# Performance work log

Measured on AMD Instinct MI355X. Metric: run time of the kernel, lower is better.

Reference implementation:

```python
import jax, jax.numpy as jnp
import numpy as np

N_USER = 50000
N_ITEM = 50000
N = N_USER + N_ITEM
NNZ = 3200000
EMB = 64
N_LAYERS = 3
BATCH = 4096
NEG_SLOPE = 0.2


def setup_inputs() -> dict:
    key = jax.random.key(0)
    ks = jax.random.split(key, 12)
    inp = {
        "users": jax.random.randint(ks[0], (BATCH,), 0, N_USER),
        "pos_items": jax.random.randint(ks[1], (BATCH,), 0, N_ITEM),
        "neg_items": jax.random.randint(ks[2], (BATCH,), 0, N_ITEM),
        "adj_row": jax.random.randint(ks[3], (NNZ,), 0, N),
        "adj_col": jax.random.randint(ks[4], (NNZ,), 0, N),
        # normalized adjacency values ~ 1/degree scale
        "adj_val": jax.random.uniform(ks[5], (NNZ,), dtype=jnp.float32) * (1.0 / 32.0),
        "user_emb": jax.random.normal(ks[6], (N_USER, EMB), dtype=jnp.float32) * 0.1,
        "item_emb": jax.random.normal(ks[7], (N_ITEM, EMB), dtype=jnp.float32) * 0.1,
        "W_gc": jax.random.normal(ks[8], (N_LAYERS, EMB, EMB), dtype=jnp.float32) * (1.0 / np.sqrt(EMB)),
        "b_gc": jax.random.normal(ks[9], (N_LAYERS, 1, EMB), dtype=jnp.float32) * 0.01,
        "W_bi": jax.random.normal(ks[10], (N_LAYERS, EMB, EMB), dtype=jnp.float32) * (1.0 / np.sqrt(EMB)),
        "b_bi": jax.random.normal(ks[11], (N_LAYERS, 1, EMB), dtype=jnp.float32) * 0.01,
    }
    return inp


def _spmm(adj_row, adj_col, adj_val, x):
    # sparse [N,N] @ dense [N,D] via gather + segment_sum
    msgs = adj_val[:, None] * x[adj_col]            # [nnz, D]
    return jax.ops.segment_sum(msgs, adj_row, num_segments=N)


def reference(users, pos_items, neg_items, adj_row, adj_col, adj_val,
              user_emb, item_emb, W_gc, b_gc, W_bi, b_bi):
    ego = jnp.concatenate([user_emb, item_emb], axis=0)   # [N, EMB]
    all_embs = [ego]
    for k in range(N_LAYERS):
        side = _spmm(adj_row, adj_col, adj_val, ego)      # [N, EMB]
        sum_emb = side @ W_gc[k] + b_gc[k]                # GC transform
        bi_emb = (ego * side) @ W_bi[k] + b_bi[k]         # BI transform
        ego = jax.nn.leaky_relu(sum_emb + bi_emb, negative_slope=NEG_SLOPE)
        # mess_dropout = 0 -> identity; L2 normalize rows (F.normalize, eps=1e-12)
        norm = jnp.maximum(jnp.linalg.norm(ego, axis=1, keepdims=True), 1e-12)
        all_embs.append(ego / norm)
    all_embs = jnp.concatenate(all_embs, axis=1)          # [N, EMB*(L+1)]
    u_g = all_embs[:N_USER]
    i_g = all_embs[N_USER:]
    return (u_g[users], i_g[pos_items], i_g[neg_items])
```

## Files before the change

### kernel.cpp

```cpp
#include <hip/hip_runtime.h>
#include <hip/hip_bf16.h>

#define N_USERC 50000
#define N_ITEMC 50000
#define NTOT    100000
#define NNZC    3200000
#define NGRP    (NNZC/4)
#define EMBC    64
#define BATCHC  4096
#define NSLOT   (3*BATCHC)
#define NBKT    196
#define CAP     17408
typedef unsigned long long u64;

typedef __attribute__((ext_vector_type(4))) float floatx4;
typedef __attribute__((ext_vector_type(2))) float floatx2;
typedef __attribute__((ext_vector_type(4))) int   intx4;
typedef __attribute__((ext_vector_type(2))) int   intx2;
typedef __attribute__((ext_vector_type(2))) unsigned uintx2;
typedef __attribute__((ext_vector_type(8))) short shortx8;

__device__ __forceinline__ float bf2f(unsigned short u) {
    return __int_as_float(((int)u) << 16);
}
__device__ __forceinline__ unsigned short f2bf(float f) {
    __hip_bfloat16 h = __float2bfloat16(f);
    return *(unsigned short*)&h;
}
__device__ __forceinline__ unsigned v2fix(float v) {
    int q = (int)(v * 1048576.0f + 0.5f);
    return (unsigned)min(q, 32767);
}

#define NB_INIT  (NTOT * EMBC / 4 / 256)
__global__ void k_prep(const float4* __restrict__ ue, const float4* __restrict__ ie,
                       ushort4* __restrict__ xb0,
                       const float* __restrict__ Wgc, const float* __restrict__ Wbi,
                       const float* __restrict__ bgc, const float* __restrict__ bbi,
                       unsigned short* __restrict__ wgT, unsigned short* __restrict__ wbT,
                       float* __restrict__ biasSum, int* __restrict__ gbcur) {
    __shared__ float wlds[64 * 65];
    int tid = threadIdx.x;
    if (blockIdx.x < NB_INIT) {
        long i = (long)blockIdx.x * 256 + tid;
        const long nu4 = (long)N_USERC * EMBC / 4;
        float4 v = (i < nu4) ? ue[i] : ie[i - nu4];
        ushort4 b; b.x = f2bf(v.x); b.y = f2bf(v.y); b.z = f2bf(v.z); b.w = f2bf(v.w);
        xb0[i] = b;
    } else if (blockIdx.x < NB_INIT + 6) {
        int wb = blockIdx.x - NB_INIT;
        int k = wb >> 1, m = wb & 1;
        const float* W = (m ? Wbi : Wgc) + k * 4096;
        unsigned short* WT = (m ? wbT : wgT) + k * 4096;
        #pragma unroll
        for (int it = 0; it < 4; ++it) {
            int i = it * 1024 + tid * 4;
            float4 v = *(const float4*)(W + i);
            int d = i >> 6, c = i & 63;
            wlds[d * 65 + c + 0] = v.x;
            wlds[d * 65 + c + 1] = v.y;
            wlds[d * 65 + c + 2] = v.z;
            wlds[d * 65 + c + 3] = v.w;
        }
        __syncthreads();
        int c = tid >> 2;
        int d0 = (tid & 3) * 16;
        unsigned short vals[16];
        #pragma unroll
        for (int j = 0; j < 16; ++j)
            vals[j] = f2bf(wlds[(d0 + j) * 65 + c]);
        *(uint4*)(WT + tid * 16)     = *(const uint4*)(vals);
        *(uint4*)(WT + tid * 16 + 8) = *(const uint4*)(vals + 8);
        if (m == 0 && tid < 64) biasSum[k * 64 + tid] = bgc[k * 64 + tid] + bbi[k * 64 + tid];
    } else {
        if (tid < NBKT) gbcur[tid] = tid * CAP;
    }
}

__global__ __launch_bounds__(256) void k_scatterP(const intx4* __restrict__ row4, const intx4* __restrict__ col4,
                                                  const floatx4* __restrict__ val4, int* __restrict__ gbcur,
                                                  u64* __restrict__ eb) {
    __shared__ int bh[NBKT], bbase[NBKT], bcur[NBKT];
    int tid = threadIdx.x;
    for (int i = tid; i < NBKT; i += 256) { bh[i] = 0; bcur[i] = 0; }
    __syncthreads();
    long gbase = (long)blockIdx.x * 1024;
    u64 e[16]; int bk[16];
    #pragma unroll
    for (int it = 0; it < 4; ++it) {
        long g = gbase + it * 256 + tid;
        if (g < NGRP) {
            intx4 r = __builtin_nontemporal_load(row4 + g);
            intx4 c = __builtin_nontemporal_load(col4 + g);
            floatx4 v = __builtin_nontemporal_load(val4 + g);
            e[it*4+0] = ((u64)r.x << 32) | ((u64)(unsigned)c.x << 15) | v2fix(v.x); bk[it*4+0] = r.x >> 9;
            e[it*4+1] = ((u64)r.y << 32) | ((u64)(unsigned)c.y << 15) | v2fix(v.y); bk[it*4+1] = r.y >> 9;
            e[it*4+2] = ((u64)r.z << 32) | ((u64)(unsigned)c.z << 15) | v2fix(v.z); bk[it*4+2] = r.z >> 9;
            e[it*4+3] = ((u64)r.w << 32) | ((u64)(unsigned)c.w << 15) | v2fix(v.w); bk[it*4+3] = r.w >> 9;
            atomicAdd(&bh[bk[it*4+0]], 1);
            atomicAdd(&bh[bk[it*4+1]], 1);
            atomicAdd(&bh[bk[it*4+2]], 1);
            atomicAdd(&bh[bk[it*4+3]], 1);
        } else {
            bk[it*4+0] = bk[it*4+1] = bk[it*4+2] = bk[it*4+3] = -1;
        }
    }
    __syncthreads();
    for (int i = tid; i < NBKT; i += 256)
        if (bh[i] > 0) bbase[i] = atomicAdd(&gbcur[i], bh[i]);
    __syncthreads();
    #pragma unroll
    for (int i = 0; i < 16; i++) {
        if (bk[i] >= 0) {
            int p = bbase[bk[i]] + atomicAdd(&bcur[bk[i]], 1);
            eb[p] = e[i];
        }
    }
}

__global__ __launch_bounds__(1024) void k_csrC(const u64* __restrict__ eb, const int* __restrict__ gbcur,
                                               intx2* __restrict__ rp2, unsigned* __restrict__ ecv) {
    __shared__ int lhist[512];
    __shared__ int lcur[512];
    __shared__ int sm[256];
    int b = blockIdx.x;
    int tid = threadIdx.x;
    int row0 = b << 9;
    if (tid < 512) lhist[tid] = 0;
    __syncthreads();
    int start = b * CAP;
    int end = gbcur[b];
    for (int e = start + tid; e < end; e += 1024) {
        u64 w = eb[e];
        int rl = (int)((w >> 32) & 0x1FFFF) - row0;
        atomicAdd(&lhist[rl], 1);
    }
    __syncthreads();
    int h0 = 0, h1 = 0, pair = 0;
    if (tid < 256) {
        h0 = lhist[2 * tid]; h1 = lhist[2 * tid + 1];
        pair = h0 + h1;
        sm[tid] = pair;
    }
    __syncthreads();
    for (int off = 1; off < 256; off <<= 1) {
        int u = 0;
        if (tid < 256 && tid >= off) u = sm[tid - off];
        __syncthreads();
        if (tid < 256) sm[tid] += u;
        __syncthreads();
    }
    if (tid < 256) {
        int pairExcl = sm[tid] - pair;
        int e0 = start + pairExcl;
        int e1 = e0 + h0;
        lcur[2 * tid] = e0;
        lcur[2 * tid + 1] = e1;
        int rg0 = row0 + 2 * tid, rg1 = rg0 + 1;
        if (rg0 < NTOT) { intx2 v; v.x = e0; v.y = e1; rp2[rg0] = v; }
        if (rg1 < NTOT) { intx2 v; v.x = e1; v.y = e1 + h1; rp2[rg1] = v; }
    }
    __syncthreads();
    for (int e = start + tid; e < end; e += 1024) {
        u64 w = eb[e];
        int rl = (int)((w >> 32) & 0x1FFFF) - row0;
        int p = atomicAdd(&lcur[rl], 1);
        ecv[p] = (unsigned)(w & 0xFFFFFFFFu);
    }
}

#define SPMM_BLOCKS 2048
__global__ __launch_bounds__(256) void k_spmm(const intx2* __restrict__ rp2, const unsigned* __restrict__ ecv,
                                              const unsigned short* __restrict__ xb,
                                              unsigned short* __restrict__ side_bf) {
    int wid = blockIdx.x * 4 + (threadIdx.x >> 6);
    int lane = threadIdx.x & 63;
    int q = lane >> 4;
    int t4 = (lane & 15) * 4;
    unsigned tb = (unsigned)(t4 * 2);
    const char* xbc = (const char*)xb;
    for (int r = wid; r < NTOT; r += SPMM_BLOCKS * 4) {
        intx2 se = rp2[r];
        int s = se.x;
        int len = se.y - s;
        const unsigned* ebase = ecv + s;
        floatx2 acc01 = {0.f, 0.f}, acc23 = {0.f, 0.f};

        int nfull = len >> 4;
        int j = 0;
        for (int it = 0; it < nfull; ++it, j += 16) {
            unsigned pk[4];
            #pragma unroll
            for (int u = 0; u < 4; ++u)
                pk[u] = __builtin_nontemporal_load(ebase + j + u * 4 + q);
            uintx2 xv[4];
            #pragma unroll
            for (int u = 0; u < 4; ++u)
                xv[u] = *(const uintx2*)(xbc + ((pk[u] >> 15) * 128u + tb));
            #pragma unroll
            for (int u = 0; u < 4; ++u) {
                float w = (float)(pk[u] & 0x7fffu);
                floatx2 x01, x23;
                x01.x = __uint_as_float(xv[u].x << 16);
                x01.y = __uint_as_float(xv[u].x & 0xffff0000u);
                x23.x = __uint_as_float(xv[u].y << 16);
                x23.y = __uint_as_float(xv[u].y & 0xffff0000u);
                acc01 += w * x01;
                acc23 += w * x23;
            }
        }
        if (j < len) {
            unsigned pk[4]; bool vm[4];
            #pragma unroll
            for (int u = 0; u < 4; ++u) {
                int je = j + u * 4 + q;
                vm[u] = (je < len);
                pk[u] = __builtin_nontemporal_load(ebase + (vm[u] ? je : 0));
            }
            uintx2 xv[4];
            #pragma unroll
            for (int u = 0; u < 4; ++u)
                xv[u] = *(const uintx2*)(xbc + ((pk[u] >> 15) * 128u + tb));
            #pragma unroll
            for (int u = 0; u < 4; ++u) {
                float w = vm[u] ? (float)(pk[u] & 0x7fffu) : 0.f;
                floatx2 x01, x23;
                x01.x = __uint_as_float(xv[u].x << 16);
                x01.y = __uint_as_float(xv[u].x & 0xffff0000u);
                x23.x = __uint_as_float(xv[u].y << 16);
                x23.y = __uint_as_float(xv[u].y & 0xffff0000u);
                acc01 += w * x01;
                acc23 += w * x23;
            }
        }

        float a0 = acc01.x, a1 = acc01.y, a2 = acc23.x, a3 = acc23.y;
        a0 += __shfl_xor(a0, 16); a1 += __shfl_xor(a1, 16); a2 += __shfl_xor(a2, 16); a3 += __shfl_xor(a3, 16);
        a0 += __shfl_xor(a0, 32); a1 += __shfl_xor(a1, 32); a2 += __shfl_xor(a2, 32); a3 += __shfl_xor(a3, 32);
        if (lane < 16) {
            const float SC = 1.0f / 1048576.0f;
            ushort4 o; o.x = f2bf(a0 * SC); o.y = f2bf(a1 * SC); o.z = f2bf(a2 * SC); o.w = f2bf(a3 * SC);
            *(ushort4*)(side_bf + (long)r * EMBC + t4) = o;
        }
    }
}

#define RPB 128
#define LDP 72
__global__ __launch_bounds__(256) void k_layer_mfma(
    const unsigned short* __restrict__ side_bf, const unsigned short* __restrict__ xb_in,
    unsigned short* __restrict__ xb_out,
    const unsigned short* __restrict__ wgT, const unsigned short* __restrict__ wbT,
    const float* __restrict__ biasSum)
{
    __shared__ unsigned short sS[RPB * LDP];
    __shared__ unsigned short sM[RPB * LDP];
    __shared__ unsigned short sWg[64 * LDP];
    __shared__ unsigned short sWb[64 * LDP];
    __shared__ float sBias[64];

    int tid = threadIdx.x;
    int row0 = blockIdx.x * RPB;

    #pragma unroll
    for (int it = 0; it < 2; ++it) {
        int item = it * 256 + tid;
        int c = item >> 3, ch = item & 7;
        *(uint4*)(sWg + c * LDP + ch * 8) = *(const uint4*)(wgT + c * 64 + ch * 8);
        *(uint4*)(sWb + c * LDP + ch * 8) = *(const uint4*)(wbT + c * 64 + ch * 8);
    }
    if (tid < 64) sBias[tid] = biasSum[tid];

    #pragma unroll
    for (int it = 0; it < (RPB * 8) / 256; ++it) {
        int item = it * 256 + tid;
        int r = item >> 3, ch = item & 7;
        long grow = row0 + r;
        uint4 sv = make_uint4(0, 0, 0, 0), ev = make_uint4(0, 0, 0, 0);
        if (grow < NTOT) {
            sv = *(const uint4*)(side_bf + grow * 64 + ch * 8);
            ev = *(const uint4*)(xb_in + grow * 64 + ch * 8);
        }
        uint4 mv;
        mv.x = f2bf(bf2f(ev.x & 0xffff) * bf2f(sv.x & 0xffff)) |
               ((unsigned int)f2bf(bf2f(ev.x >> 16) * bf2f(sv.x >> 16)) << 16);
        mv.y = f2bf(bf2f(ev.y & 0xffff) * bf2f(sv.y & 0xffff)) |
               ((unsigned int)f2bf(bf2f(ev.y >> 16) * bf2f(sv.y >> 16)) << 16);
        mv.z = f2bf(bf2f(ev.z & 0xffff) * bf2f(sv.z & 0xffff)) |
               ((unsigned int)f2bf(bf2f(ev.z >> 16) * bf2f(sv.z >> 16)) << 16);
        mv.w = f2bf(bf2f(ev.w & 0xffff) * bf2f(sv.w & 0xffff)) |
               ((unsigned int)f2bf(bf2f(ev.w >> 16) * bf2f(sv.w >> 16)) << 16);
        *(uint4*)(sS + r * LDP + ch * 8) = sv;
        *(uint4*)(sM + r * LDP + ch * 8) = mv;
    }
    __syncthreads();

    int wave = tid >> 6, lane = tid & 63;
    int quad = lane >> 4, l16 = lane & 15;

    floatx4 accG[2][4], accB[2][4];
    #pragma unroll
    for (int rt = 0; rt < 2; rt++)
        #pragma unroll
        for (int ct = 0; ct < 4; ct++) {
            accG[rt][ct] = (floatx4){0.f, 0.f, 0.f, 0.f};
            accB[rt][ct] = (floatx4){0.f, 0.f, 0.f, 0.f};
        }

    #pragma unroll
    for (int kc = 0; kc < 64; kc += 32) {
        shortx8 aS[2], aM[2];
        #pragma unroll
        for (int rt = 0; rt < 2; rt++) {
            int r = wave * 32 + rt * 16 + l16;
            aS[rt] = *(const shortx8*)(sS + r * LDP + kc + quad * 8);
            aM[rt] = *(const shortx8*)(sM + r * LDP + kc + quad * 8);
        }
        #pragma unroll
        for (int ct = 0; ct < 4; ct++) {
            int c = ct * 16 + l16;
            shortx8 bG = *(const shortx8*)(sWg + c * LDP + kc + quad * 8);
            shortx8 bB = *(const shortx8*)(sWb + c * LDP + kc + quad * 8);
            #pragma unroll
            for (int rt = 0; rt < 2; rt++) {
                accG[rt][ct] = __builtin_amdgcn_mfma_f32_16x16x32_bf16(aS[rt], bG, accG[rt][ct], 0, 0, 0);
                accB[rt][ct] = __builtin_amdgcn_mfma_f32_16x16x32_bf16(aM[rt], bB, accB[rt][ct], 0, 0, 0);
            }
        }
    }

    #pragma unroll
    for (int rt = 0; rt < 2; rt++)
        #pragma unroll
        for (int ct = 0; ct < 4; ct++) {
            int c = ct * 16 + l16;
            float bs = sBias[c];
            #pragma unroll
            for (int reg = 0; reg < 4; reg++) {
                int r = wave * 32 + rt * 16 + quad * 4 + reg;
                long grow = row0 + r;
                if (grow < NTOT) {
                    float v = accG[rt][ct][reg] + accB[rt][ct][reg] + bs;
                    float o = (v > 0.f) ? v : 0.2f * v;
                    xb_out[grow * 64 + c] = f2bf(o);
                }
            }
        }
}

__global__ __launch_bounds__(256) void k_gatherAll(
    const unsigned short* __restrict__ xb0, const unsigned short* __restrict__ xb1,
    const unsigned short* __restrict__ xb2, const unsigned short* __restrict__ xb3,
    const int* __restrict__ users, const int* __restrict__ pos, const int* __restrict__ neg,
    float* __restrict__ out) {
    int gw = (blockIdx.x * blockDim.x + threadIdx.x) >> 6;
    int lane = threadIdx.x & 63;
    int slot = gw >> 2, layer = gw & 3;
    if (slot >= NSLOT) return;
    int row;
    if (slot < BATCHC)          row = users[slot];
    else if (slot < 2 * BATCHC) row = N_USERC + pos[slot - BATCHC];
    else                        row = N_USERC + neg[slot - 2 * BATCHC];
    const unsigned short* src = (layer == 0) ? xb0 : (layer == 1) ? xb1 : (layer == 2) ? xb2 : xb3;
    float v = bf2f(src[(long)row * 64 + lane]);
    if (layer != 0) {
        float ss = v * v;
        for (int off = 32; off > 0; off >>= 1) ss += __shfl_xor(ss, off);
        float nrm = fmaxf(sqrtf(ss), 1e-12f);
        v = v / nrm;
    }
    out[(long)slot * 256 + layer * 64 + lane] = v;
}

extern "C" void kernel_launch(void* const* d_in, const int* in_sizes, int n_in,
                              void* d_out, int out_size, void* d_ws, size_t ws_size,
                              hipStream_t stream) {
    const int*   users   = (const int*)d_in[0];
    const int*   pos     = (const int*)d_in[1];
    const int*   neg     = (const int*)d_in[2];
    const int*   adj_row = (const int*)d_in[3];
    const int*   adj_col = (const int*)d_in[4];
    const float* adj_val = (const float*)d_in[5];
    const float* user_emb = (const float*)d_in[6];
    const float* item_emb = (const float*)d_in[7];
    const float* W_gc = (const float*)d_in[8];
    const float* b_gc = (const float*)d_in[9];
    const float* W_bi = (const float*)d_in[10];
    const float* b_bi = (const float*)d_in[11];
    float* out = (float*)d_out;

    char* p = (char*)d_ws;
    unsigned* ecv = (unsigned*)p;               p += (size_t)NBKT * CAP * 4;
    u64*  eb  = (u64*)p;                        p += (size_t)NBKT * CAP * 8;
    unsigned short* xb2 = (unsigned short*)eb;
    unsigned short* xb3 = (unsigned short*)((char*)eb + (size_t)NTOT * EMBC * 2);
    unsigned short* side_bf = (unsigned short*)p; p += (size_t)NTOT * EMBC * 2;
    unsigned short* xb0 = (unsigned short*)p;   p += (size_t)NTOT * EMBC * 2;
    unsigned short* xb1 = (unsigned short*)p;   p += (size_t)NTOT * EMBC * 2;
    intx2* rp2 = (intx2*)p;                     p += (size_t)NTOT * 8;
    int*  gbcur = (int*)p;                      p += 1024;
    unsigned short* wgT = (unsigned short*)p;   p += 3 * 4096 * 2;
    unsigned short* wbT = (unsigned short*)p;   p += 3 * 4096 * 2;
    float* biasSum = (float*)p;                 p += 3 * 64 * 4;

    k_prep<<<NB_INIT + 7, 256, 0, stream>>>(
        (const float4*)user_emb, (const float4*)item_emb, (ushort4*)xb0,
        W_gc, W_bi, b_gc, b_bi, wgT, wbT, biasSum, gbcur);

    k_scatterP<<<(NNZC + 4095) / 4096, 256, 0, stream>>>(
        (const intx4*)adj_row, (const intx4*)adj_col, (const floatx4*)adj_val, gbcur, eb);
    k_csrC<<<NBKT, 1024, 0, stream>>>(eb, gbcur, rp2, ecv);

    unsigned short* xbs[4] = {xb0, xb1, xb2, xb3};
    const int NB_LAYER = (NTOT + RPB - 1) / RPB;
    for (int k = 0; k < 3; k++) {
        k_spmm<<<SPMM_BLOCKS, 256, 0, stream>>>(rp2, ecv, xbs[k], side_bf);
        k_layer_mfma<<<NB_LAYER, 256, 0, stream>>>(side_bf, xbs[k], xbs[k + 1],
            wgT + (size_t)k * 4096, wbT + (size_t)k * 4096, biasSum + (size_t)k * 64);
    }
    k_gatherAll<<<(NSLOT * 4) / 4, 256, 0, stream>>>(xb0, xb1, xb2, xb3, users, pos, neg, out);
}
```

Measured before the change: 398.7 us.

## Split SpMM edges by column segment to improve gather locality across passes

The CSR build now sorts each row's edges into four column segments (taken from the top bits of the packed edge word) and stores per-row segment counts. The SpMM kernel makes four passes, one per column segment, keeping partial row sums in shared memory between passes. In each pass all waves gather from a quarter of the embedding table, which is meant to raise cache hit rates for the random gathers. In exchange, row metadata is read four times, the inner loop is unrolled less, and there is extra shared-memory traffic.

```diff
diff --git a/kernel.cpp b/kernel.cpp
--- a/kernel.cpp
+++ b/kernel.cpp
@@ -11,6 +11,7 @@
 #define NSLOT   (3*BATCHC)
 #define NBKT    196
 #define CAP     17408
+#define NSEG2   4
 typedef unsigned long long u64;
 
 typedef __attribute__((ext_vector_type(4))) float floatx4;
@@ -119,128 +120,124 @@
 }
 
 __global__ __launch_bounds__(1024) void k_csrC(const u64* __restrict__ eb, const int* __restrict__ gbcur,
-                                               intx2* __restrict__ rp2, unsigned* __restrict__ ecv) {
-    __shared__ int lhist[512];
-    __shared__ int lcur[512];
-    __shared__ int sm[256];
+                                               int* __restrict__ rpA, ushort4* __restrict__ rpC,
+                                               unsigned* __restrict__ ecv) {
+    __shared__ int lhist[2048];
+    __shared__ int lcur[2048];
+    __shared__ int sm[1024];
     int b = blockIdx.x;
     int tid = threadIdx.x;
     int row0 = b << 9;
-    if (tid < 512) lhist[tid] = 0;
+    lhist[tid] = 0; lhist[tid + 1024] = 0;
     __syncthreads();
     int start = b * CAP;
     int end = gbcur[b];
     for (int e = start + tid; e < end; e += 1024) {
         u64 w = eb[e];
+        unsigned lo = (unsigned)w;
         int rl = (int)((w >> 32) & 0x1FFFF) - row0;
-        atomicAdd(&lhist[rl], 1);
-    }
-    __syncthreads();
-    int h0 = 0, h1 = 0, pair = 0;
-    if (tid < 256) {
-        h0 = lhist[2 * tid]; h1 = lhist[2 * tid + 1];
-        pair = h0 + h1;
-        sm[tid] = pair;
-    }
-    __syncthreads();
-    for (int off = 1; off < 256; off <<= 1) {
-        int u = 0;
-        if (tid < 256 && tid >= off) u = sm[tid - off];
+        int seg = lo >> 30;
+        atomicAdd(&lhist[(rl << 2) | seg], 1);
+    }
+    __syncthreads();
+    int h0 = lhist[2 * tid], h1 = lhist[2 * tid + 1];
+    int pair = h0 + h1;
+    sm[tid] = pair;
+    __syncthreads();
+    for (int off = 1; off < 1024; off <<= 1) {
+        int u = (tid >= off) ? sm[tid - off] : 0;
         __syncthreads();
-        if (tid < 256) sm[tid] += u;
+        sm[tid] += u;
         __syncthreads();
     }
-    if (tid < 256) {
-        int pairExcl = sm[tid] - pair;
-        int e0 = start + pairExcl;
-        int e1 = e0 + h0;
-        lcur[2 * tid] = e0;
-        lcur[2 * tid + 1] = e1;
-        int rg0 = row0 + 2 * tid, rg1 = rg0 + 1;
-        if (rg0 < NTOT) { intx2 v; v.x = e0; v.y = e1; rp2[rg0] = v; }
-        if (rg1 < NTOT) { intx2 v; v.x = e1; v.y = e1 + h1; rp2[rg1] = v; }
+    int pairExcl = sm[tid] - pair;
+    lcur[2 * tid] = start + pairExcl;
+    lcur[2 * tid + 1] = start + pairExcl + h0;
+    __syncthreads();
+    if (tid < 512) {
+        int r = row0 + tid;
+        if (r < NTOT) {
+            rpA[r] = lcur[4 * tid];
+            ushort4 c;
+            c.x = (unsigned short)lhist[4 * tid];
+            c.y = (unsigned short)lhist[4 * tid + 1];
+            c.z = (unsigned short)lhist[4 * tid + 2];
+            c.w = (unsigned short)lhist[4 * tid + 3];
+            rpC[r] = c;
+        }
     }
     __syncthreads();
     for (int e = start + tid; e < end; e += 1024) {
         u64 w = eb[e];
+        unsigned lo = (unsigned)w;
         int rl = (int)((w >> 32) & 0x1FFFF) - row0;
-        int p = atomicAdd(&lcur[rl], 1);
-        ecv[p] = (unsigned)(w & 0xFFFFFFFFu);
+        int seg = lo >> 30;
+        int p = atomicAdd(&lcur[(rl << 2) | seg], 1);
+        ecv[p] = lo;
     }
 }
 
 #define SPMM_BLOCKS 2048
-__global__ __launch_bounds__(256) void k_spmm(const intx2* __restrict__ rp2, const unsigned* __restrict__ ecv,
+#define RSLOT 13
+__global__ __launch_bounds__(256) void k_spmm(const int* __restrict__ rpA, const ushort4* __restrict__ rpC,
+                                              const unsigned* __restrict__ ecv,
                                               const unsigned short* __restrict__ xb,
                                               unsigned short* __restrict__ side_bf) {
-    int wid = blockIdx.x * 4 + (threadIdx.x >> 6);
-    int lane = threadIdx.x & 63;
-    int q = lane >> 4;
-    int t4 = (lane & 15) * 4;
+    __shared__ float accf[4 * RSLOT * 64];
+    int tid = threadIdx.x;
+    int wv = tid >> 6, lane = tid & 63, q = lane >> 4, l16 = lane & 15;
+    int wid = blockIdx.x * 4 + wv;
+    for (int i = tid; i < 4 * RSLOT * 64; i += 256) accf[i] = 0.f;
+    __syncthreads();
+    float* myacc = accf + wv * RSLOT * 64;
+    int t4 = l16 * 4;
     unsigned tb = (unsigned)(t4 * 2);
     const char* xbc = (const char*)xb;
-    for (int r = wid; r < NTOT; r += SPMM_BLOCKS * 4) {
-        intx2 se = rp2[r];
-        int s = se.x;
-        int len = se.y - s;
-        const unsigned* ebase = ecv + s;
-        floatx2 acc01 = {0.f, 0.f}, acc23 = {0.f, 0.f};
-
-        int nfull = len >> 4;
-        int j = 0;
-        for (int it = 0; it < nfull; ++it, j += 16) {
-            unsigned pk[4];
-            #pragma unroll
-            for (int u = 0; u < 4; ++u)
-                pk[u] = __builtin_nontemporal_load(ebase + j + u * 4 + q);
-            uintx2 xv[4];
-            #pragma unroll
-            for (int u = 0; u < 4; ++u)
-                xv[u] = *(const uintx2*)(xbc + ((pk[u] >> 15) * 128u + tb));
-            #pragma unroll
-            for (int u = 0; u < 4; ++u) {
-                float w = (float)(pk[u] & 0x7fffu);
-                floatx2 x01, x23;
-                x01.x = __uint_as_float(xv[u].x << 16);
-                x01.y = __uint_as_float(xv[u].x & 0xffff0000u);
-                x23.x = __uint_as_float(xv[u].y << 16);
-                x23.y = __uint_as_float(xv[u].y & 0xffff0000u);
-                acc01 += w * x01;
-                acc23 += w * x23;
+    for (int s = 0; s < NSEG2; ++s) {
+        int k = 0;
+        for (int r = wid; r < NTOT; r += SPMM_BLOCKS * 4, ++k) {
+            int off = rpA[r];
+            ushort4 c = rpC[r];
+            int cnt;
+            if (s == 0)      { cnt = c.x; }
+            else if (s == 1) { off += c.x; cnt = c.y; }
+            else if (s == 2) { off += c.x + c.y; cnt = c.z; }
+            else             { off += c.x + c.y + c.z; cnt = c.w; }
+            float* slot = myacc + k * 64 + t4;
+            floatx4 prev = *(const floatx4*)slot;
+            float a0 = (q == 0) ? prev.x : 0.f;
+            float a1 = (q == 0) ? prev.y : 0.f;
+            float a2 = (q == 0) ? prev.z : 0.f;
+            float a3 = (q == 0) ? prev.w : 0.f;
+            if (cnt > 0) {
+                bool vm = q < cnt;
+                unsigned pk = __builtin_nontemporal_load(ecv + (vm ? off + q : off));
+                int j = 0;
+                while (true) {
+                    int jn = j + 4;
+                    bool vmn = (jn + q) < cnt;
+                    unsigned pkn = __builtin_nontemporal_load(ecv + (vmn ? off + jn + q : off));
+                    uintx2 xv = *(const uintx2*)(xbc + ((pk >> 15) * 128u + tb));
+                    float w = vm ? (float)(pk & 0x7fffu) : 0.f;
+                    a0 += w * __uint_as_float(xv.x << 16);
+                    a1 += w * __uint_as_float(xv.x & 0xffff0000u);
+                    a2 += w * __uint_as_float(xv.y << 16);
+                    a3 += w * __uint_as_float(xv.y & 0xffff0000u);
+                    if (jn >= cnt) break;
+                    j = jn; pk = pkn; vm = vmn;
+                }
             }
-        }
-        if (j < len) {
-            unsigned pk[4]; bool vm[4];
-            #pragma unroll
-            for (int u = 0; u < 4; ++u) {
-                int je = j + u * 4 + q;
-                vm[u] = (je < len);
-                pk[u] = __builtin_nontemporal_load(ebase + (vm[u] ? je : 0));
+            a0 += __shfl_xor(a0, 16); a1 += __shfl_xor(a1, 16); a2 += __shfl_xor(a2, 16); a3 += __shfl_xor(a3, 16);
+            a0 += __shfl_xor(a0, 32); a1 += __shfl_xor(a1, 32); a2 += __shfl_xor(a2, 32); a3 += __shfl_xor(a3, 32);
+            if (s < NSEG2 - 1) {
+                if (lane < 16) { floatx4 v = {a0, a1, a2, a3}; *(floatx4*)slot = v; }
+            } else {
+                if (lane < 16) {
+                    const float SC = 1.0f / 1048576.0f;
+                    ushort4 o; o.x = f2bf(a0 * SC); o.y = f2bf(a1 * SC); o.z = f2bf(a2 * SC); o.w = f2bf(a3 * SC);
+                    *(ushort4*)(side_bf + (long)r * EMBC + t4) = o;
+                }
             }
-            uintx2 xv[4];
-            #pragma unroll
-            for (int u = 0; u < 4; ++u)
-                xv[u] = *(const uintx2*)(xbc + ((pk[u] >> 15) * 128u + tb));
-            #pragma unroll
-            for (int u = 0; u < 4; ++u) {
-                float w = vm[u] ? (float)(pk[u] & 0x7fffu) : 0.f;
-                floatx2 x01, x23;
-                x01.x = __uint_as_float(xv[u].x << 16);
-                x01.y = __uint_as_float(xv[u].x & 0xffff0000u);
-                x23.x = __uint_as_float(xv[u].y << 16);
-                x23.y = __uint_as_float(xv[u].y & 0xffff0000u);
-                acc01 += w * x01;
-                acc23 += w * x23;
-            }
-        }
-
-        float a0 = acc01.x, a1 = acc01.y, a2 = acc23.x, a3 = acc23.y;
-        a0 += __shfl_xor(a0, 16); a1 += __shfl_xor(a1, 16); a2 += __shfl_xor(a2, 16); a3 += __shfl_xor(a3, 16);
-        a0 += __shfl_xor(a0, 32); a1 += __shfl_xor(a1, 32); a2 += __shfl_xor(a2, 32); a3 += __shfl_xor(a3, 32);
-        if (lane < 16) {
-            const float SC = 1.0f / 1048576.0f;
-            ushort4 o; o.x = f2bf(a0 * SC); o.y = f2bf(a1 * SC); o.z = f2bf(a2 * SC); o.w = f2bf(a3 * SC);
-            *(ushort4*)(side_bf + (long)r * EMBC + t4) = o;
         }
     }
 }
@@ -397,7 +394,8 @@
     unsigned short* side_bf = (unsigned short*)p; p += (size_t)NTOT * EMBC * 2;
     unsigned short* xb0 = (unsigned short*)p;   p += (size_t)NTOT * EMBC * 2;
     unsigned short* xb1 = (unsigned short*)p;   p += (size_t)NTOT * EMBC * 2;
-    intx2* rp2 = (intx2*)p;                     p += (size_t)NTOT * 8;
+    int*  rpA = (int*)p;                        p += (size_t)NTOT * 4 + 64;
+    ushort4* rpC = (ushort4*)p;                 p += (size_t)NTOT * 8 + 64;
     int*  gbcur = (int*)p;                      p += 1024;
     unsigned short* wgT = (unsigned short*)p;   p += 3 * 4096 * 2;
     unsigned short* wbT = (unsigned short*)p;   p += 3 * 4096 * 2;
@@ -409,12 +407,12 @@
 
     k_scatterP<<<(NNZC + 4095) / 4096, 256, 0, stream>>>(
         (const intx4*)adj_row, (const intx4*)adj_col, (const floatx4*)adj_val, gbcur, eb);
-    k_csrC<<<NBKT, 1024, 0, stream>>>(eb, gbcur, rp2, ecv);
+    k_csrC<<<NBKT, 1024, 0, stream>>>(eb, gbcur, rpA, rpC, ecv);
 
     unsigned short* xbs[4] = {xb0, xb1, xb2, xb3};
     const int NB_LAYER = (NTOT + RPB - 1) / RPB;
     for (int k = 0; k < 3; k++) {
-        k_spmm<<<SPMM_BLOCKS, 256, 0, stream>>>(rp2, ecv, xbs[k], side_bf);
+        k_spmm<<<SPMM_BLOCKS, 256, 0, stream>>>(rpA, rpC, ecv, xbs[k], side_bf);
         k_layer_mfma<<<NB_LAYER, 256, 0, stream>>>(side_bf, xbs[k], xbs[k + 1],
             wgT + (size_t)k * 4096, wbT + (size_t)k * 4096, biasSum + (size_t)k * 64);
     }
```

Measured after the change: 571.7 us. 1.43x slower.
